# Kernel optimization log

Measured on AMD Instinct MI355X. Metric: run time of the kernel, lower is better.

The kernel has to match this reference:

```python
import jax, jax.numpy as jnp
import numpy as np

N, E = 50000, 1600000
CIN, H, EA, NT, EMB = 128, 64, 16, 16, 8
EPS = 1e-5


def _sage(x, src, dst, Wl, bl, Wr, n):
    # PyG SAGEConv (mean aggr): out = lin_l(mean_{j in N(i)} x_j) + lin_r(x_i)
    s = jax.ops.segment_sum(x[src], dst, num_segments=n)            # [N,C]
    cnt = jax.ops.segment_sum(jnp.ones((src.shape[0], 1), x.dtype), dst, num_segments=n)
    agg = s / jnp.maximum(cnt, 1.0)
    return agg @ Wl.T + bl + x @ Wr.T


def _bn(x, g, b):
    # BatchNorm1d, training-mode (batch statistics, biased variance)
    m = x.mean(axis=0)
    v = x.var(axis=0)
    return g * (x - m) * jax.lax.rsqrt(v + EPS) + b


def setup_inputs() -> dict:
    key = jax.random.key(0)
    ks = jax.random.split(key, 24)
    r = lambda k, shp, s=0.1: (jax.random.normal(k, shp, dtype=jnp.float32) * s)
    inp = {
        "x": jax.random.normal(ks[0], (N, CIN), dtype=jnp.float32),
        "edge_index": jax.random.randint(ks[1], (2, E), 0, N, dtype=jnp.int64),
        "edge_attr": jax.random.normal(ks[2], (E, EA), dtype=jnp.float32),
        "type_idx": jax.random.randint(ks[3], (E,), 0, NT, dtype=jnp.int64),
        "type_emb": r(ks[4], (NT, EMB)),
        "W1l": r(ks[5], (H, CIN)), "b1l": jnp.zeros((H,), jnp.float32), "W1r": r(ks[6], (H, CIN)),
        "g1": jnp.ones((H,), jnp.float32), "be1": jnp.zeros((H,), jnp.float32),
        "W2l": r(ks[7], (H, H)), "b2l": jnp.zeros((H,), jnp.float32), "W2r": r(ks[8], (H, H)),
        "g2": jnp.ones((H,), jnp.float32), "be2": jnp.zeros((H,), jnp.float32),
        "Wm1": r(ks[9], (H, 2 * H + EA + EMB)), "bm1": jnp.zeros((H,), jnp.float32),
        "Wm2": r(ks[10], (H // 2, H)), "bm2": jnp.zeros((H // 2,), jnp.float32),
        "Wm3": r(ks[11], (2, H // 2)), "bm3": jnp.zeros((2,), jnp.float32),
    }
    return inp


def reference(x, edge_index, edge_attr, type_idx, type_emb,
              W1l, b1l, W1r, g1, be1,
              W2l, b2l, W2r, g2, be2,
              Wm1, bm1, Wm2, bm2, Wm3, bm3):
    src, dst = edge_index[0], edge_index[1]
    n = x.shape[0]
    h = jax.nn.relu(_bn(_sage(x, src, dst, W1l, b1l, W1r, n), g1, be1))
    h = jax.nn.relu(_bn(_sage(h, src, dst, W2l, b2l, W2r, n), g2, be2))
    # edge feature construction: gather-concat  [E, 2H+EA+EMB]
    e = jnp.concatenate([h[src], h[dst], edge_attr, type_emb[type_idx]], axis=1)
    z = jax.nn.relu(e @ Wm1.T + bm1)            # dropout = identity (eval)
    z = jax.nn.relu(z @ Wm2.T + bm2)
    return z @ Wm3.T + bm3                       # [E, 2]
```

## Files before the change

kernel.cpp:

```cpp
#include <hip/hip_runtime.h>

constexpr float BN_EPS = 1e-5f;

typedef __attribute__((ext_vector_type(8))) short bf16x8;
typedef __attribute__((ext_vector_type(4))) float f32x4;

__device__ __forceinline__ float4 ld4(const float* p) { return *(const float4*)p; }
__device__ __forceinline__ unsigned short f2bf(float x) {
  union { float f; unsigned u; } c; c.f = x;
  unsigned r = (c.u + 0x7fffu + ((c.u >> 16) & 1u)) >> 16;
  return (unsigned short)r;
}
__device__ __forceinline__ float bf1(unsigned short h) {
  union { unsigned i; float f; } a; a.i = ((unsigned)h) << 16; return a.f;
}
__device__ __forceinline__ float2 bf2(unsigned u) {
  union { unsigned i; float f; } lo, hi;
  lo.i = u << 16; hi.i = u & 0xffff0000u;
  return make_float2(lo.f, hi.f);
}
__device__ __forceinline__ unsigned pk_bf16(float lo, float hi) {
  unsigned r;
  asm("v_cvt_pk_bf16_f32 %0, %1, %2" : "=v"(r) : "v"(lo), "v"(hi));
  return r;
}

__global__ __launch_bounds__(256) void csr_count_kernel(const int* __restrict__ dst, int E, int SL,
                                                        int* __restrict__ cntT) {
  __shared__ int c[256];
  c[threadIdx.x] = 0;
  __syncthreads();
  const int s = blockIdx.x;
  const int e0 = s * SL;
  const int e1 = min(E, e0 + SL);
  for (int e = e0 + threadIdx.x; e < e1; e += 256)
    atomicAdd(&c[dst[e] >> 8], 1);
  __syncthreads();
  cntT[threadIdx.x * 256 + s] = c[threadIdx.x];
}

__global__ __launch_bounds__(1024) void scan_blocks_kernel(const int* __restrict__ deg, int n,
                                                           int* __restrict__ off, int* __restrict__ bsum) {
  __shared__ int lds[1024];
  int i = blockIdx.x * 1024 + threadIdx.x;
  int v = (i < n) ? deg[i] : 0;
  lds[threadIdx.x] = v;
  __syncthreads();
  for (int s = 1; s < 1024; s <<= 1) {
    int t = (threadIdx.x >= (unsigned)s) ? lds[threadIdx.x - s] : 0;
    __syncthreads();
    lds[threadIdx.x] += t;
    __syncthreads();
  }
  if (i < n) off[i] = lds[threadIdx.x] - v;
  if (threadIdx.x == 1023) bsum[blockIdx.x] = lds[1023];
}

__global__ void scan_sums_kernel(int* __restrict__ bsum, int nb) {
  int carry = 0;
  for (int base = 0; base < nb; base += 64) {
    int l = base + (int)threadIdx.x;
    int orig = (l < nb) ? bsum[l] : 0;
    int v = orig;
    for (int s = 1; s < 64; s <<= 1) {
      int t = __shfl_up(v, s);
      if ((int)threadIdx.x >= s) v += t;
    }
    if (l < nb) bsum[l] = carry + v - orig;
    carry += __shfl(v, 63);
  }
}

__global__ __launch_bounds__(1024) void scan_add_kernel(const int* __restrict__ bsum, int n,
                                                        int* __restrict__ off, int* __restrict__ cur) {
  int i = blockIdx.x * 1024 + threadIdx.x;
  if (i < n) {
    int o = off[i] + bsum[blockIdx.x];
    off[i] = o;
    cur[i] = o;
  }
}

__global__ __launch_bounds__(256) void csr_part_kernel(const int* __restrict__ src,
                                                       const int* __restrict__ dst, int E, int SL,
                                                       const int* __restrict__ base,
                                                       unsigned* __restrict__ pairs) {
  __shared__ int curL[256];
  const int s = blockIdx.x;
  curL[threadIdx.x] = base[threadIdx.x * 256 + s];
  __syncthreads();
  const int e0 = s * SL;
  const int e1 = min(E, e0 + SL);
  for (int e = e0 + threadIdx.x; e < e1; e += 256) {
    int d = dst[e];
    int sr = src[e];
    int p = atomicAdd(&curL[d >> 8], 1);
    pairs[p] = (unsigned)sr | ((unsigned)(d & 255) << 16);
  }
}

__global__ __launch_bounds__(256) void csr_fill_kernel(const unsigned* __restrict__ pairs,
                                                       const int* __restrict__ base, int n,
                                                       int* __restrict__ deg, int* __restrict__ off,
                                                       int* __restrict__ elist) {
  __shared__ int degL[256], scanL[256], curL[256];
  const int b = blockIdx.x;
  const int p0 = base[b * 256];
  const int p1 = base[(b + 1) * 256];
  degL[threadIdx.x] = 0;
  __syncthreads();
  for (int p = p0 + threadIdx.x; p < p1; p += 256)
    atomicAdd(&degL[(pairs[p] >> 16) & 255], 1);
  __syncthreads();
  int v = degL[threadIdx.x];
  scanL[threadIdx.x] = v;
  __syncthreads();
  for (int st = 1; st < 256; st <<= 1) {
    int t = (threadIdx.x >= (unsigned)st) ? scanL[threadIdx.x - st] : 0;
    __syncthreads();
    scanL[threadIdx.x] += t;
    __syncthreads();
  }
  int excl = scanL[threadIdx.x] - v;
  curL[threadIdx.x] = excl;
  int node = b * 256 + threadIdx.x;
  if (node < n) { deg[node] = v; off[node] = p0 + excl; }
  __syncthreads();
  for (int p = p0 + threadIdx.x; p < p1; p += 256) {
    unsigned pk = pairs[p];
    int q = atomicAdd(&curL[(pk >> 16) & 255], 1);
    elist[p0 + q] = (int)(pk & 0xffffu);
  }
}

template <int K, bool BN, int MODE>
__global__ __launch_bounds__(256) void proj3_kernel(
    const float* __restrict__ X,
    const float* __restrict__ Wa, int lda, int koffa,
    const float* __restrict__ Wb, int ldb, int koffb,
    const float* __restrict__ scale, const float* __restrict__ shift,
    void* __restrict__ outA, void* __restrict__ outB, int n) {
  constexpr int KP = K + 4;
  __shared__ alignas(16) unsigned short ws[64 * KP];
  __shared__ alignas(16) unsigned short xs[64 * KP];
  const int ob = blockIdx.y;
  const float* W = ob ? Wb : Wa;
  const int ld = ob ? ldb : lda;
  const int koff = ob ? koffb : koffa;
  const int tid = threadIdx.x;

  for (int idx = tid; idx < 64 * K; idx += 256) {
    int o = idx / K, k = idx - o * K;
    ws[o * KP + k] = f2bf(W[o * ld + koff + k]);
  }
  const int nb = blockIdx.x * 64;
  for (int idx = tid; idx < 64 * K; idx += 256) {
    int nl = idx / K, k = idx - nl * K;
    int node = nb + nl;
    float v = (node < n) ? X[(size_t)node * K + k] : 0.f;
    if (BN) v = fmaxf(fmaf(v, scale[k], shift[k]), 0.f);
    xs[nl * KP + k] = f2bf(v);
  }
  __syncthreads();

  const int w = tid >> 6, lane = tid & 63;
  const int g = lane >> 4, c16 = lane & 15;

  f32x4 acc[4];
#pragma unroll
  for (int ct = 0; ct < 4; ++ct) acc[ct] = f32x4{0.f, 0.f, 0.f, 0.f};

  const unsigned short* xrow = &xs[(w * 16 + c16) * KP];
#pragma unroll
  for (int ks = 0; ks < K / 32; ++ks) {
    union { bf16x8 v; uint2 u[2]; } a;
    a.u[0] = *(const uint2*)(xrow + ks * 32 + g * 8);
    a.u[1] = *(const uint2*)(xrow + ks * 32 + g * 8 + 4);
#pragma unroll
    for (int ct = 0; ct < 4; ++ct) {
      union { bf16x8 v; uint2 u[2]; } b;
      const unsigned short* wrow = &ws[(ct * 16 + c16) * KP + ks * 32 + g * 8];
      b.u[0] = *(const uint2*)(wrow);
      b.u[1] = *(const uint2*)(wrow + 4);
      acc[ct] = __builtin_amdgcn_mfma_f32_16x16x32_bf16(a.v, b.v, acc[ct], 0, 0, 0);
    }
  }

#pragma unroll
  for (int ct = 0; ct < 4; ++ct) {
    int col = ct * 16 + c16;
#pragma unroll
    for (int r = 0; r < 4; ++r) {
      int node = nb + w * 16 + g * 4 + r;
      if (node < n) {
        float v = acc[ct][r];
        if (MODE == 0) {
          if (ob == 0) ((unsigned short*)outA)[(size_t)node * 64 + col] = f2bf(v);
          else         ((float*)outB)[(size_t)node * 64 + col] = v;
        } else {
          ((unsigned short*)outA)[(size_t)node * 128 + ob * 64 + col] = f2bf(v);
        }
      }
    }
  }
}

__global__ __launch_bounds__(256) void agg_kernel(
    const unsigned short* __restrict__ Pm, const float* __restrict__ Xr,
    const int* __restrict__ off, const int* __restrict__ deg,
    const int* __restrict__ elist, const float* __restrict__ bl,
    float* __restrict__ HP, float* __restrict__ partials, int n) {
  int node = blockIdx.x * 4 + (threadIdx.x >> 6);
  int c = threadIdx.x & 63;
  float hpv = 0.f;
  if (node < n) {
    int d = deg[node];
    int o = off[node];
    float a0 = 0.f, a1 = 0.f, a2 = 0.f, a3 = 0.f;
    float a4 = 0.f, a5 = 0.f, a6 = 0.f, a7 = 0.f;
    int j = 0;
    for (; j + 8 <= d; j += 8) {
      int s0 = elist[o + j + 0], s1 = elist[o + j + 1], s2 = elist[o + j + 2], s3 = elist[o + j + 3];
      int s4 = elist[o + j + 4], s5 = elist[o + j + 5], s6 = elist[o + j + 6], s7 = elist[o + j + 7];
      a0 += bf1(Pm[(size_t)s0 * 64 + c]);
      a1 += bf1(Pm[(size_t)s1 * 64 + c]);
      a2 += bf1(Pm[(size_t)s2 * 64 + c]);
      a3 += bf1(Pm[(size_t)s3 * 64 + c]);
      a4 += bf1(Pm[(size_t)s4 * 64 + c]);
      a5 += bf1(Pm[(size_t)s5 * 64 + c]);
      a6 += bf1(Pm[(size_t)s6 * 64 + c]);
      a7 += bf1(Pm[(size_t)s7 * 64 + c]);
    }
    for (; j < d; ++j) a0 += bf1(Pm[(size_t)elist[o + j] * 64 + c]);
    float acc = ((a0 + a1) + (a2 + a3)) + ((a4 + a5) + (a6 + a7));
    float agg = acc / (float)(d > 0 ? d : 1);
    size_t idx = (size_t)node * 64 + c;
    hpv = agg + bl[c] + Xr[idx];
    HP[idx] = hpv;
  }
  __shared__ float ls[256], lq[256];
  ls[threadIdx.x] = hpv;
  lq[threadIdx.x] = hpv * hpv;
  __syncthreads();
  if (threadIdx.x < 64) {
    float s = ls[threadIdx.x] + ls[threadIdx.x + 64] + ls[threadIdx.x + 128] + ls[threadIdx.x + 192];
    float q = lq[threadIdx.x] + lq[threadIdx.x + 64] + lq[threadIdx.x + 128] + lq[threadIdx.x + 192];
    int slot = (blockIdx.x & 31) * 128;
    atomicAdd(&partials[slot + c], s);
    atomicAdd(&partials[slot + 64 + c], q);
  }
}

__global__ void bn_finalize_kernel(const float* __restrict__ partials, int nblk, int n,
                                   const float* __restrict__ g, const float* __restrict__ be,
                                   float* __restrict__ scale, float* __restrict__ shift) {
  int c = threadIdx.x;
  float s = 0.f, q = 0.f;
  for (int b = 0; b < nblk; ++b) { s += partials[b * 128 + c]; q += partials[b * 128 + 64 + c]; }
  float mean = s / (float)n;
  float var = q / (float)n - mean * mean;
  float sc = g[c] * rsqrtf(var + BN_EPS);
  scale[c] = sc;
  shift[c] = be[c] - mean * sc;
}

__global__ void prep_kernel(const float* __restrict__ Wm1, const float* __restrict__ temb,
                            const float* __restrict__ bm1, const float* __restrict__ Wm2,
                            unsigned short* __restrict__ blob) {
  for (int i = threadIdx.x; i < 2048; i += 256) {
    int o = i >> 5, k = i & 31;
    float v;
    if (k < 16) {
      v = Wm1[o * 152 + 128 + k];
    } else {
      int t = k - 16;
      v = bm1[o];
#pragma unroll
      for (int q = 0; q < 8; ++q) v = fmaf(Wm1[o * 152 + 144 + q], temb[t * 8 + q], v);
    }
    blob[o * 32 + k] = f2bf(v);
  }
  for (int i = threadIdx.x; i < 2048; i += 256) {
    int j = i >> 6, k = i & 63;
    blob[2048 + j * 64 + k] = f2bf(Wm2[j * 64 + k]);
  }
}

struct RawA { uint4 r0, r1; };
struct UVfr { uint4 u0, u1, v0, v1; };

__global__ __launch_bounds__(64, 4) void edge_mfma_kernel(
    const unsigned short* __restrict__ UVb, const int* __restrict__ ei,
    const float* __restrict__ eattr, const int* __restrict__ tix,
    const unsigned short* __restrict__ blob,
    const float* __restrict__ Wm3, const float* __restrict__ bm2,
    const float* __restrict__ bm3, float* __restrict__ out, int E) {
  constexpr int P = 66;
  __shared__ unsigned short z1T[64 * P];
  unsigned* z1T32 = (unsigned*)z1T;

  const int tid = threadIdx.x;
  const int g = tid >> 4, c16 = tid & 15;
  const int base = blockIdx.x * 64;

  bf16x8 bfr[4];
#pragma unroll
  for (int ct = 0; ct < 4; ++ct)
    bfr[ct] = *(const bf16x8*)(blob + (ct * 16 + c16) * 32 + g * 8);
  bf16x8 bw[2][2];
  const unsigned short* w2b = blob + 2048;
#pragma unroll
  for (int jt = 0; jt < 2; ++jt)
#pragma unroll
    for (int ks = 0; ks < 2; ++ks)
      bw[jt][ks] = *(const bf16x8*)(w2b + (jt * 16 + c16) * 64 + ks * 32 + g * 8);
  union { bf16x8 v; short s8[8]; } bi0, bi1;
#pragma unroll
  for (int j = 0; j < 8; ++j) {
    bi0.s8[j] = (g * 8 + j == c16) ? (short)0x3F80 : (short)0;
    bi1.s8[j] = (g * 8 + j == 16 + c16) ? (short)0x3F80 : (short)0;
  }
  const float bm2c0 = bm2[c16], bm2c1 = bm2[16 + c16];
  const float2 w3c0 = make_float2(Wm3[c16], Wm3[32 + c16]);
  const float2 w3c1 = make_float2(Wm3[16 + c16], Wm3[48 + c16]);
  const float b3a = bm3[0], b3b = bm3[1];

  int sA[4], dA[4];
  bool lvA[4];
#pragma unroll
  for (int et = 0; et < 4; ++et) {
    int erow = base + et * 16 + c16;
    lvA[et] = erow < E;
    sA[et] = lvA[et] ? ei[erow] : 0;
    dA[et] = lvA[et] ? ei[E + erow] : 0;
  }

  auto load_a = [&](int et) -> RawA {
    RawA ra;
    int erow = base + et * 16 + c16;
    if (g < 2) {
      if (lvA[et]) {
        const uint4* eap = (const uint4*)(eattr + (size_t)erow * 16 + g * 8);
        ra.r0 = eap[0];
        ra.r1 = eap[1];
      } else {
        ra.r0 = make_uint4(0, 0, 0, 0);
        ra.r1 = make_uint4(0, 0, 0, 0);
      }
    } else {
      ra.r0.x = (unsigned)(lvA[et] ? tix[erow] : -1);
    }
    return ra;
  };
  auto gather_uv = [&](int et) -> UVfr {
    const uint4* ur = (const uint4*)(UVb + (size_t)sA[et] * 128);
    const uint4* vr = (const uint4*)(UVb + (size_t)dA[et] * 128);
    UVfr x;
    x.u0 = ur[g];
    x.u1 = ur[4 + g];
    x.v0 = vr[8 + g];
    x.v1 = vr[12 + g];
    return x;
  };
  auto compute = [&](int et, const RawA& ra, const UVfr& uv) {
    bf16x8 a_eaoh;
    if (g < 2) {
      union { uint4 u; float4 f; } c0, c1;
      c0.u = ra.r0; c1.u = ra.r1;
      union { bf16x8 v; unsigned u[4]; } cc;
      cc.u[0] = pk_bf16(c0.f.x, c0.f.y); cc.u[1] = pk_bf16(c0.f.z, c0.f.w);
      cc.u[2] = pk_bf16(c1.f.x, c1.f.y); cc.u[3] = pk_bf16(c1.f.z, c1.f.w);
      a_eaoh = cc.v;
    } else {
      int t = (int)ra.r0.x;
      int kb = (g - 2) * 8;
      union { bf16x8 v; short s8[8]; } cc;
#pragma unroll
      for (int j = 0; j < 8; ++j) cc.s8[j] = (t == kb + j) ? (short)0x3F80 : (short)0;
      a_eaoh = cc.v;
    }
    union { uint4 u; bf16x8 v; } au0, au1, av0, av1;
    au0.u = uv.u0; au1.u = uv.u1; av0.u = uv.v0; av1.u = uv.v1;
#pragma unroll
    for (int ct = 0; ct < 4; ++ct) {
      f32x4 acc = {0.f, 0.f, 0.f, 0.f};
      acc = __builtin_amdgcn_mfma_f32_16x16x32_bf16(a_eaoh, bfr[ct], acc, 0, 0, 0);
      const bf16x8 au = (ct < 2) ? au0.v : au1.v;
      const bf16x8 av = (ct < 2) ? av0.v : av1.v;
      const bf16x8 bi = (ct & 1) ? bi1.v : bi0.v;
      acc = __builtin_amdgcn_mfma_f32_16x16x32_bf16(au, bi, acc, 0, 0, 0);
      acc = __builtin_amdgcn_mfma_f32_16x16x32_bf16(av, bi, acc, 0, 0, 0);
      int cw = (ct * 16 + c16) * 33 + et * 8 + g * 2;
      z1T32[cw]     = pk_bf16(fmaxf(acc[0], 0.f), fmaxf(acc[1], 0.f));
      z1T32[cw + 1] = pk_bf16(fmaxf(acc[2], 0.f), fmaxf(acc[3], 0.f));
    }
  };

  RawA ra0 = load_a(0);
  UVfr uv0 = gather_uv(0);
  RawA ra1 = load_a(1);
  UVfr uv1 = gather_uv(1);
  compute(0, ra0, uv0);
  ra0 = load_a(2);
  uv0 = gather_uv(2);
  compute(1, ra1, uv1);
  ra1 = load_a(3);
  uv1 = gather_uv(3);
  compute(2, ra0, uv0);
  compute(3, ra1, uv1);
  __syncthreads();

#pragma unroll
  for (int et = 0; et < 4; ++et) {
    int ecol = et * 16 + c16;
    union { bf16x8 v; unsigned short s8[8]; } A0, A1;
#pragma unroll
    for (int j = 0; j < 8; ++j) {
      A0.s8[j] = z1T[(g * 8 + j) * P + ecol];
      A1.s8[j] = z1T[(32 + g * 8 + j) * P + ecol];
    }
    f32x4 p0 = {0.f, 0.f, 0.f, 0.f}, p1 = {0.f, 0.f, 0.f, 0.f};
#pragma unroll
    for (int jt = 0; jt < 2; ++jt) {
      float bm = jt ? bm2c1 : bm2c0;
      float2 w3 = jt ? w3c1 : w3c0;
      f32x4 acc = {bm, bm, bm, bm};
      acc = __builtin_amdgcn_mfma_f32_16x16x32_bf16(A0.v, bw[jt][0], acc, 0, 0, 0);
      acc = __builtin_amdgcn_mfma_f32_16x16x32_bf16(A1.v, bw[jt][1], acc, 0, 0, 0);
#pragma unroll
      for (int r = 0; r < 4; ++r) {
        float z = fmaxf(acc[r], 0.f);
        p0[r] = fmaf(z, w3.x, p0[r]);
        p1[r] = fmaf(z, w3.y, p1[r]);
      }
    }
#pragma unroll
    for (int m = 1; m < 16; m <<= 1) {
#pragma unroll
      for (int r = 0; r < 4; ++r) {
        p0[r] += __shfl_xor(p0[r], m, 16);
        p1[r] += __shfl_xor(p1[r], m, 16);
      }
    }
    if (c16 == 0) {
      int eo = base + et * 16 + g * 4;
      if (eo + 3 < E) {
        float4 f0 = make_float4(p0[0] + b3a, p1[0] + b3b, p0[1] + b3a, p1[1] + b3b);
        float4 f1 = make_float4(p0[2] + b3a, p1[2] + b3b, p0[3] + b3a, p1[3] + b3b);
        *(float4*)&out[(size_t)eo * 2] = f0;
        *(float4*)&out[(size_t)eo * 2 + 4] = f1;
      } else {
#pragma unroll
        for (int r = 0; r < 4; ++r) {
          if (eo + r < E) {
            out[(size_t)(eo + r) * 2] = p0[r] + b3a;
            out[(size_t)(eo + r) * 2 + 1] = p1[r] + b3b;
          }
        }
      }
    }
  }
}

extern "C" void kernel_launch(void* const* d_in, const int* in_sizes, int n_in,
                              void* d_out, int out_size, void* d_ws, size_t ws_size,
                              hipStream_t stream) {
  const float* x    = (const float*)d_in[0];
  const int*   ei   = (const int*)d_in[1];
  const float* ea   = (const float*)d_in[2];
  const int*   tix  = (const int*)d_in[3];
  const float* temb = (const float*)d_in[4];
  const float* W1l  = (const float*)d_in[5];
  const float* b1l  = (const float*)d_in[6];
  const float* W1r  = (const float*)d_in[7];
  const float* g1   = (const float*)d_in[8];
  const float* be1  = (const float*)d_in[9];
  const float* W2l  = (const float*)d_in[10];
  const float* b2l  = (const float*)d_in[11];
  const float* W2r  = (const float*)d_in[12];
  const float* g2   = (const float*)d_in[13];
  const float* be2  = (const float*)d_in[14];
  const float* Wm1  = (const float*)d_in[15];
  const float* bm1  = (const float*)d_in[16];
  const float* Wm2  = (const float*)d_in[17];
  const float* bm2  = (const float*)d_in[18];
  const float* Wm3  = (const float*)d_in[19];
  const float* bm3  = (const float*)d_in[20];
  float* out = (float*)d_out;

  const int N = in_sizes[0] / 128;
  const int E = in_sizes[3];

  char* w = (char*)d_ws;
  auto alloc = [&](size_t bytes) -> char* {
    char* p = w;
    w += (bytes + 255) & ~(size_t)255;
    return p;
  };
  int* deg   = (int*)alloc((size_t)N * 4);
  int* off   = (int*)alloc((size_t)(N + 1) * 4);
  int* elist = (int*)alloc((size_t)E * 4);
  unsigned short* Pm  = (unsigned short*)alloc((size_t)N * 64 * 2);
  float*          Xr  = (float*)alloc((size_t)N * 64 * 4);
  unsigned short* UVb = (unsigned short*)alloc((size_t)N * 128 * 2);
  float* HP       = (float*)alloc((size_t)N * 64 * 4);
  float* partials = (float*)alloc(32 * 128 * 4);
  float* sc1 = (float*)alloc(64 * 4);
  float* sh1 = (float*)alloc(64 * 4);
  float* sc2 = (float*)alloc(64 * 4);
  float* sh2 = (float*)alloc(64 * 4);
  unsigned short* blob = (unsigned short*)alloc(4096 * 2);
  int* cntT = (int*)alloc(65536 * 4);
  int* base = (int*)alloc((65536 + 256) * 4);
  int* bsum = (int*)alloc(256 * 4);
  unsigned* pairs = (unsigned*)Pm;

  const int* srcp = ei;
  const int* dstp = ei + E;

  const int SL = (E + 255) / 256;
  const int NB = (N + 255) >> 8;
  int nb4 = (N + 3) / 4;
  int nb64 = (N + 63) / 64;

  hipLaunchKernelGGL(csr_count_kernel, dim3(256), dim3(256), 0, stream, dstp, E, SL, cntT);
  hipLaunchKernelGGL(scan_blocks_kernel, dim3(64), dim3(1024), 0, stream, cntT, 65536, base, bsum);
  hipLaunchKernelGGL(scan_sums_kernel, dim3(1), dim3(64), 0, stream, bsum, 64);
  hipLaunchKernelGGL(scan_add_kernel, dim3(64), dim3(1024), 0, stream, bsum, 65536, base, base);
  hipLaunchKernelGGL(csr_part_kernel, dim3(256), dim3(256), 0, stream, srcp, dstp, E, SL, base, pairs);
  hipLaunchKernelGGL(csr_fill_kernel, dim3(NB), dim3(256), 0, stream, pairs, base, N, deg, off, elist);

  hipLaunchKernelGGL((proj3_kernel<128, false, 0>), dim3(nb64, 2), dim3(256), 0, stream,
                     x, W1l, 128, 0, W1r, 128, 0, (const float*)nullptr, (const float*)nullptr,
                     (void*)Pm, (void*)Xr, N);
  hipMemsetAsync(partials, 0, 32 * 128 * 4, stream);
  hipLaunchKernelGGL(agg_kernel, dim3(nb4), dim3(256), 0, stream,
                     Pm, Xr, off, deg, elist, b1l, HP, partials, N);
  hipLaunchKernelGGL(bn_finalize_kernel, dim3(1), dim3(64), 0, stream, partials, 32, N, g1, be1, sc1, sh1);

  hipLaunchKernelGGL((proj3_kernel<64, true, 0>), dim3(nb64, 2), dim3(256), 0, stream,
                     HP, W2l, 64, 0, W2r, 64, 0, sc1, sh1, (void*)Pm, (void*)Xr, N);
  hipMemsetAsync(partials, 0, 32 * 128 * 4, stream);
  hipLaunchKernelGGL(agg_kernel, dim3(nb4), dim3(256), 0, stream,
                     Pm, Xr, off, deg, elist, b2l, HP, partials, N);
  hipLaunchKernelGGL(bn_finalize_kernel, dim3(1), dim3(64), 0, stream, partials, 32, N, g2, be2, sc2, sh2);

  hipLaunchKernelGGL((proj3_kernel<64, true, 1>), dim3(nb64, 2), dim3(256), 0, stream,
                     HP, Wm1, 152, 0, Wm1, 152, 64, sc2, sh2, (void*)UVb, (void*)nullptr, N);
  hipLaunchKernelGGL(prep_kernel, dim3(1), dim3(256), 0, stream, Wm1, temb, bm1, Wm2, blob);

  int ebm = (E + 63) / 64;
  hipLaunchKernelGGL(edge_mfma_kernel, dim3(ebm), dim3(64), 0, stream,
                     UVb, ei, ea, tix, blob, Wm3, bm2, bm3, out, E);
}
```

Before: 338.7 us.

## Split projected features into column halves and aggregate each half separately

The projection kernel now writes the bf16 neighbour-projection matrix as two planar halves of 32 columns each. Aggregation runs as two launches, one per half. In each launch a wavefront splits a node's edge list between its two 32-lane halves and combines them with a shuffle. The aim is to shrink each pass's gather working set (half the rows' bytes) so it fits in cache better, at the cost of reading the edge list twice and an extra launch. Each gather row becomes 64 bytes, so memory transactions may be used less efficiently.

Result: slower. 383.6 us (+13.2%).

```diff
diff --git a/kernel.cpp b/kernel.cpp
--- a/kernel.cpp
+++ b/kernel.cpp
@@ -195,8 +195,12 @@
       if (node < n) {
         float v = acc[ct][r];
         if (MODE == 0) {
-          if (ob == 0) ((unsigned short*)outA)[(size_t)node * 64 + col] = f2bf(v);
-          else         ((float*)outB)[(size_t)node * 64 + col] = v;
+          if (ob == 0) {
+            size_t half_off = (size_t)(col >> 5) * ((size_t)n * 32);
+            ((unsigned short*)outA)[half_off + (size_t)node * 32 + (col & 31)] = f2bf(v);
+          } else {
+            ((float*)outB)[(size_t)node * 64 + col] = v;
+          }
         } else {
           ((unsigned short*)outA)[(size_t)node * 128 + ob * 64 + col] = f2bf(v);
         }
@@ -205,49 +209,50 @@
   }
 }
 
-__global__ __launch_bounds__(256) void agg_kernel(
-    const unsigned short* __restrict__ Pm, const float* __restrict__ Xr,
+template <int H>
+__global__ __launch_bounds__(256) void agg2_kernel(
+    const unsigned short* __restrict__ PmH, const float* __restrict__ Xr,
     const int* __restrict__ off, const int* __restrict__ deg,
     const int* __restrict__ elist, const float* __restrict__ bl,
     float* __restrict__ HP, float* __restrict__ partials, int n) {
   int node = blockIdx.x * 4 + (threadIdx.x >> 6);
-  int c = threadIdx.x & 63;
+  int lane = threadIdx.x & 63;
+  int c = lane & 31;
+  int pe = lane >> 5;
   float hpv = 0.f;
   if (node < n) {
     int d = deg[node];
     int o = off[node];
     float a0 = 0.f, a1 = 0.f, a2 = 0.f, a3 = 0.f;
-    float a4 = 0.f, a5 = 0.f, a6 = 0.f, a7 = 0.f;
-    int j = 0;
-    for (; j + 8 <= d; j += 8) {
-      int s0 = elist[o + j + 0], s1 = elist[o + j + 1], s2 = elist[o + j + 2], s3 = elist[o + j + 3];
-      int s4 = elist[o + j + 4], s5 = elist[o + j + 5], s6 = elist[o + j + 6], s7 = elist[o + j + 7];
-      a0 += bf1(Pm[(size_t)s0 * 64 + c]);
-      a1 += bf1(Pm[(size_t)s1 * 64 + c]);
-      a2 += bf1(Pm[(size_t)s2 * 64 + c]);
-      a3 += bf1(Pm[(size_t)s3 * 64 + c]);
-      a4 += bf1(Pm[(size_t)s4 * 64 + c]);
-      a5 += bf1(Pm[(size_t)s5 * 64 + c]);
-      a6 += bf1(Pm[(size_t)s6 * 64 + c]);
-      a7 += bf1(Pm[(size_t)s7 * 64 + c]);
-    }
-    for (; j < d; ++j) a0 += bf1(Pm[(size_t)elist[o + j] * 64 + c]);
-    float acc = ((a0 + a1) + (a2 + a3)) + ((a4 + a5) + (a6 + a7));
-    float agg = acc / (float)(d > 0 ? d : 1);
-    size_t idx = (size_t)node * 64 + c;
-    hpv = agg + bl[c] + Xr[idx];
-    HP[idx] = hpv;
+    int j = pe;
+    for (; j + 6 < d; j += 8) {
+      int s0 = elist[o + j], s1 = elist[o + j + 2];
+      int s2 = elist[o + j + 4], s3 = elist[o + j + 6];
+      a0 += bf1(PmH[(size_t)s0 * 32 + c]);
+      a1 += bf1(PmH[(size_t)s1 * 32 + c]);
+      a2 += bf1(PmH[(size_t)s2 * 32 + c]);
+      a3 += bf1(PmH[(size_t)s3 * 32 + c]);
+    }
+    for (; j < d; j += 2) a0 += bf1(PmH[(size_t)elist[o + j] * 32 + c]);
+    float acc = (a0 + a1) + (a2 + a3);
+    acc += __shfl_xor(acc, 32);
+    if (pe == 0) {
+      float agg = acc / (float)(d > 0 ? d : 1);
+      size_t idx = (size_t)node * 64 + H * 32 + c;
+      hpv = agg + bl[H * 32 + c] + Xr[idx];
+      HP[idx] = hpv;
+    }
   }
   __shared__ float ls[256], lq[256];
   ls[threadIdx.x] = hpv;
   lq[threadIdx.x] = hpv * hpv;
   __syncthreads();
-  if (threadIdx.x < 64) {
+  if (threadIdx.x < 32) {
     float s = ls[threadIdx.x] + ls[threadIdx.x + 64] + ls[threadIdx.x + 128] + ls[threadIdx.x + 192];
     float q = lq[threadIdx.x] + lq[threadIdx.x + 64] + lq[threadIdx.x + 128] + lq[threadIdx.x + 192];
     int slot = (blockIdx.x & 31) * 128;
-    atomicAdd(&partials[slot + c], s);
-    atomicAdd(&partials[slot + 64 + c], q);
+    atomicAdd(&partials[slot + H * 32 + threadIdx.x], s);
+    atomicAdd(&partials[slot + 64 + H * 32 + threadIdx.x], q);
   }
 }
 
@@ -523,6 +528,9 @@
   int nb4 = (N + 3) / 4;
   int nb64 = (N + 63) / 64;
 
+  unsigned short* Pm0 = Pm;
+  unsigned short* Pm1 = Pm + (size_t)N * 32;
+
   hipLaunchKernelGGL(csr_count_kernel, dim3(256), dim3(256), 0, stream, dstp, E, SL, cntT);
   hipLaunchKernelGGL(scan_blocks_kernel, dim3(64), dim3(1024), 0, stream, cntT, 65536, base, bsum);
   hipLaunchKernelGGL(scan_sums_kernel, dim3(1), dim3(64), 0, stream, bsum, 64);
@@ -534,15 +542,19 @@
                      x, W1l, 128, 0, W1r, 128, 0, (const float*)nullptr, (const float*)nullptr,
                      (void*)Pm, (void*)Xr, N);
   hipMemsetAsync(partials, 0, 32 * 128 * 4, stream);
-  hipLaunchKernelGGL(agg_kernel, dim3(nb4), dim3(256), 0, stream,
-                     Pm, Xr, off, deg, elist, b1l, HP, partials, N);
+  hipLaunchKernelGGL((agg2_kernel<0>), dim3(nb4), dim3(256), 0, stream,
+                     Pm0, Xr, off, deg, elist, b1l, HP, partials, N);
+  hipLaunchKernelGGL((agg2_kernel<1>), dim3(nb4), dim3(256), 0, stream,
+                     Pm1, Xr, off, deg, elist, b1l, HP, partials, N);
   hipLaunchKernelGGL(bn_finalize_kernel, dim3(1), dim3(64), 0, stream, partials, 32, N, g1, be1, sc1, sh1);
 
   hipLaunchKernelGGL((proj3_kernel<64, true, 0>), dim3(nb64, 2), dim3(256), 0, stream,
                      HP, W2l, 64, 0, W2r, 64, 0, sc1, sh1, (void*)Pm, (void*)Xr, N);
   hipMemsetAsync(partials, 0, 32 * 128 * 4, stream);
-  hipLaunchKernelGGL(agg_kernel, dim3(nb4), dim3(256), 0, stream,
-                     Pm, Xr, off, deg, elist, b2l, HP, partials, N);
+  hipLaunchKernelGGL((agg2_kernel<0>), dim3(nb4), dim3(256), 0, stream,
+                     Pm0, Xr, off, deg, elist, b2l, HP, partials, N);
+  hipLaunchKernelGGL((agg2_kernel<1>), dim3(nb4), dim3(256), 0, stream,
+                     Pm1, Xr, off, deg, elist, b2l, HP, partials, N);
   hipLaunchKernelGGL(bn_finalize_kernel, dim3(1), dim3(64), 0, stream, partials, 32, N, g2, be2, sc2, sh2);
 
   hipLaunchKernelGGL((proj3_kernel<64, true, 1>), dim3(nb64, 2), dim3(256), 0, stream,
```
